# Kernel tuning notes

Hardware: AMD Instinct MI355X
Metric: run time of the kernel (lower is better)

Reference implementation:

```python
import jax, jax.numpy as jnp
import numpy as np

NUM_EMBEDDINGS = 1024
EMBEDDING_DIM = 256
BETA = 0.25


def setup_inputs() -> dict:
    key = jax.random.key(0)
    k1, k2 = jax.random.split(key)
    inputs = jax.random.normal(k1, (32, EMBEDDING_DIM, 64, 64), dtype=jnp.float32)
    # codebook init: uniform(-1/K, 1/K), matching nn.Embedding init in the module
    embedding = jax.random.uniform(
        k2, (NUM_EMBEDDINGS, EMBEDDING_DIM), dtype=jnp.float32,
        minval=-1.0 / NUM_EMBEDDINGS, maxval=1.0 / NUM_EMBEDDINGS)
    return {"inputs": inputs, "embedding": embedding, "beta": BETA}


def reference(inputs, embedding, beta):
    # inputs: [B, D, H, W] -> [B, H, W, D]
    x = jnp.transpose(inputs, (0, 2, 3, 1))
    in_shape = x.shape
    flat = x.reshape(-1, embedding.shape[1])  # [N, D]
    dist = (jnp.sum(flat * flat, axis=1, keepdims=True)
            + jnp.sum(embedding * embedding, axis=1)
            - 2.0 * flat @ embedding.T)
    codebook_indices = jnp.argmin(dist, axis=1)  # [N]
    quantized = embedding[codebook_indices].reshape(in_shape)  # [B,H,W,D]
    sg = jax.lax.stop_gradient
    e_latent_loss = beta * jnp.mean((sg(quantized) - x) ** 2)
    q_latent_loss = jnp.mean((quantized - sg(x)) ** 2)
    loss = e_latent_loss + q_latent_loss
    # straight-through estimator
    quantized_st = x + sg(quantized - x)
    return loss, jnp.transpose(quantized_st, (0, 3, 1, 2))
```

## Files before the change

kernel.cpp:

```cpp
#include <hip/hip_runtime.h>
#include <hip/hip_bf16.h>


#define DIN 256
#define NCODES 1024
#define NTOT 33554432

typedef __attribute__((ext_vector_type(8))) short short8;
typedef __attribute__((ext_vector_type(4))) float float4v;
typedef __attribute__((ext_vector_type(4))) unsigned short ushort4v;

static __device__ __forceinline__ unsigned short f2bf(float f) {
  unsigned int u = __float_as_uint(f);
  unsigned int r = (u + 0x7fffu + ((u >> 16) & 1u)) >> 16;
  return (unsigned short)r;
}

__global__ void vq_prep(const float* __restrict__ e,
                        unsigned short* __restrict__ e_bf,
                        float* __restrict__ norms) {
  int wave = threadIdx.x >> 6, lane = threadIdx.x & 63;
  int k = blockIdx.x * 4 + wave;
  const float4v* src = (const float4v*)(e + k * DIN);
  float4v v = src[lane];
  float ss = v[0]*v[0] + v[1]*v[1] + v[2]*v[2] + v[3]*v[3];
  ushort4v pk;
  pk[0] = f2bf(v[0]); pk[1] = f2bf(v[1]); pk[2] = f2bf(v[2]); pk[3] = f2bf(v[3]);
  ((ushort4v*)(e_bf + k * DIN))[lane] = pk;
  #pragma unroll
  for (int m = 1; m < 64; m <<= 1) ss += __shfl_xor(ss, m, 64);
  if (lane == 0) norms[k] = ss;
}

__global__ void __launch_bounds__(256, 2)
vq_main(const float* __restrict__ xin, const float* __restrict__ e_fp,
        const unsigned short* __restrict__ e_bf, const float* __restrict__ norms,
        float* __restrict__ out, float* __restrict__ loss_acc) {
  __shared__ char smem[65536];
  unsigned short* xs = (unsigned short*)smem;
  unsigned short* es = (unsigned short*)smem;
  float* vs  = (float*)(smem + 49152);
  int*   is_ = (int*)  (smem + 49664);
  int*   fi  = (int*)  (smem + 50176);
  float* rs  = (float*)(smem + 50432);
  float* qs  = (float*)smem;

  const int tid  = threadIdx.x;
  const int wave = tid >> 6, lane = tid & 63;
  const int m16  = lane & 15, quad = lane >> 4;
  const int wr   = wave >> 1, wc = wave & 1;
  const int b    = blockIdx.x >> 6, h = blockIdx.x & 63;
  const int base = b * 1048576 + h * 64;

  {
    int w = lane;
    for (int q8 = 0; q8 < 8; ++q8) {
      int cc = q8 * 4 + wave;
      int d0 = cc * 8;
      short8 pk;
      #pragma unroll
      for (int ii = 0; ii < 8; ++ii) {
        float xv = xin[base + (d0 + ii) * 4096 + w];
        pk[ii] = (short)f2bf(xv);
      }
      *(short8*)(xs + w * 256 + 8 * (cc ^ (w & 7))) = pk;
    }
  }
  __syncthreads();

  short8 areg[16];
  #pragma unroll
  for (int i = 0; i < 2; ++i) {
    #pragma unroll
    for (int kk = 0; kk < 8; ++kk) {
      int r = wr * 32 + i * 16 + m16;
      int cc = kk * 4 + quad;
      areg[i * 8 + kk] = *(short8*)(xs + r * 256 + 8 * (cc ^ (r & 7)));
    }
  }
  __syncthreads();

  float bestv[2][4];
  int   besti[2][4];
  float4v acc[2][4];
  #pragma unroll
  for (int i = 0; i < 2; ++i)
    #pragma unroll
    for (int r = 0; r < 4; ++r) {
      bestv[i][r] = INFINITY; besti[i][r] = 0;
      acc[i][r] = (float4v)(0.0f);
    }

  for (int ct = 0; ct < 8; ++ct) {
    int c0 = ct * 128;
    #pragma unroll
    for (int j = 0; j < 16; ++j) {
      int f = j * 256 + tid;
      int kL = f >> 5, cc = f & 31;
      short8 vch = *(const short8*)(e_bf + (c0 + kL) * 256 + cc * 8);
      *(short8*)(es + kL * 256 + 8 * (cc ^ (kL & 7))) = vch;
    }
    __syncthreads();
    #pragma unroll
    for (int kk = 0; kk < 8; ++kk) {
      short8 bfr[4];
      #pragma unroll
      for (int j = 0; j < 4; ++j) {
        int cL = wc * 64 + j * 16 + m16;
        int cc = kk * 4 + quad;
        bfr[j] = *(short8*)(es + cL * 256 + 8 * (cc ^ (cL & 7)));
      }
      #pragma unroll
      for (int i = 0; i < 2; ++i)
        #pragma unroll
        for (int j = 0; j < 4; ++j)
          acc[i][j] = __builtin_amdgcn_mfma_f32_16x16x32_bf16(
              areg[i * 8 + kk], bfr[j], acc[i][j], 0, 0, 0);
    }
    #pragma unroll
    for (int j = 0; j < 4; ++j) {
      int col = c0 + wc * 64 + j * 16 + m16;
      float nj = norms[col];
      #pragma unroll
      for (int i = 0; i < 2; ++i) {
        #pragma unroll
        for (int r = 0; r < 4; ++r) {
          float s = nj - 2.0f * acc[i][j][r];
          if (s < bestv[i][r]) { bestv[i][r] = s; besti[i][r] = col; }
        }
        acc[i][j] = (float4v)(0.0f);
      }
    }
    __syncthreads();
  }

  #pragma unroll
  for (int msk = 1; msk <= 8; msk <<= 1) {
    #pragma unroll
    for (int i = 0; i < 2; ++i)
      #pragma unroll
      for (int r = 0; r < 4; ++r) {
        float ov = __shfl_xor(bestv[i][r], msk, 64);
        int   oi = __shfl_xor(besti[i][r], msk, 64);
        if (ov < bestv[i][r] || (ov == bestv[i][r] && oi < besti[i][r])) {
          bestv[i][r] = ov; besti[i][r] = oi;
        }
      }
  }
  if (m16 == 0) {
    #pragma unroll
    for (int i = 0; i < 2; ++i)
      #pragma unroll
      for (int r = 0; r < 4; ++r) {
        int rl = wr * 32 + i * 16 + quad * 4 + r;
        vs [rl * 2 + wc] = bestv[i][r];
        is_[rl * 2 + wc] = besti[i][r];
      }
  }
  __syncthreads();
  if (tid < 64) {
    float v0 = vs[tid * 2], v1 = vs[tid * 2 + 1];
    fi[tid] = (v1 < v0) ? is_[tid * 2 + 1] : is_[tid * 2];
  }
  __syncthreads();

  float lsum = 0.0f;
  for (int h2 = 0; h2 < 2; ++h2) {
    #pragma unroll
    for (int j = 0; j < 8; ++j) {
      int f = j * 256 + tid;
      int w2 = f >> 5, cc = f & 31;
      int idx = fi[w2];
      float4v qv = *(const float4v*)(e_fp + idx * DIN + h2 * 128 + cc * 4);
      #pragma unroll
      for (int ii = 0; ii < 4; ++ii)
        qs[(cc * 4 + ii) * 65 + w2] = qv[ii];
    }
    __syncthreads();
    for (int dd = 0; dd < 32; ++dd) {
      int dL = wave * 32 + dd;
      int g = base + (h2 * 128 + dL) * 4096 + lane;
      float q  = qs[dL * 65 + lane];
      float xv = xin[g];
      out[1 + g] = q;
      float df = q - xv;
      lsum += df * df;
    }
    __syncthreads();
  }

  #pragma unroll
  for (int msk = 1; msk < 64; msk <<= 1) lsum += __shfl_xor(lsum, msk, 64);
  if (lane == 0) rs[wave] = lsum;
  __syncthreads();
  if (tid == 0) atomicAdd(loss_acc, rs[0] + rs[1] + rs[2] + rs[3]);
}

__global__ void vq_fin(const float* __restrict__ loss_acc,
                       const float* __restrict__ beta,
                       float* __restrict__ out) {
  out[0] = (1.0f + beta[0]) * loss_acc[0] / 33554432.0f;
}

extern "C" void kernel_launch(void* const* d_in, const int* in_sizes, int n_in,
                              void* d_out, int out_size, void* d_ws, size_t ws_size,
                              hipStream_t stream) {
  const float* xin  = (const float*)d_in[0];
  const float* emb  = (const float*)d_in[1];
  const float* beta = (const float*)d_in[2];
  float* out = (float*)d_out;
  float* loss_acc = (float*)d_ws;
  float* norms = (float*)((char*)d_ws + 4096);
  unsigned short* e_bf = (unsigned short*)((char*)d_ws + 8192);

  hipMemsetAsync(d_ws, 0, 4, stream);
  vq_prep<<<256, 256, 0, stream>>>(emb, e_bf, norms);
  vq_main<<<2048, 256, 0, stream>>>(xin, emb, e_bf, norms, out, loss_acc);
  vq_fin<<<1, 1, 0, stream>>>(loss_acc, beta, out);
}
```

Before: 364.2 us.

## Chunk-major codebook layout with direct-to-LDS loads, smaller tiles for higher occupancy

```diff
diff --git a/kernel.cpp b/kernel.cpp
--- a/kernel.cpp
+++ b/kernel.cpp
@@ -4,10 +4,10 @@
 
 #define DIN 256
 #define NCODES 1024
-#define NTOT 33554432
 
 typedef __attribute__((ext_vector_type(8))) short short8;
 typedef __attribute__((ext_vector_type(4))) float float4v;
+typedef __attribute__((ext_vector_type(2))) float float2v;
 typedef __attribute__((ext_vector_type(4))) unsigned short ushort4v;
 
 static __device__ __forceinline__ unsigned short f2bf(float f) {
@@ -17,33 +17,32 @@
 }
 
 __global__ void vq_prep(const float* __restrict__ e,
-                        unsigned short* __restrict__ e_bf,
+                        unsigned short* __restrict__ e_bf2,
                         float* __restrict__ norms) {
   int wave = threadIdx.x >> 6, lane = threadIdx.x & 63;
   int k = blockIdx.x * 4 + wave;
-  const float4v* src = (const float4v*)(e + k * DIN);
-  float4v v = src[lane];
+  float4v v = ((const float4v*)(e + k * DIN))[lane];
   float ss = v[0]*v[0] + v[1]*v[1] + v[2]*v[2] + v[3]*v[3];
   ushort4v pk;
   pk[0] = f2bf(v[0]); pk[1] = f2bf(v[1]); pk[2] = f2bf(v[2]); pk[3] = f2bf(v[3]);
-  ((ushort4v*)(e_bf + k * DIN))[lane] = pk;
+  int cc = lane >> 1, sub = lane & 1;
+  *(ushort4v*)(e_bf2 + (cc * NCODES + k) * 8 + sub * 4) = pk;
   #pragma unroll
   for (int m = 1; m < 64; m <<= 1) ss += __shfl_xor(ss, m, 64);
   if (lane == 0) norms[k] = ss;
 }
 
-__global__ void __launch_bounds__(256, 2)
+__global__ void __launch_bounds__(256, 4)
 vq_main(const float* __restrict__ xin, const float* __restrict__ e_fp,
-        const unsigned short* __restrict__ e_bf, const float* __restrict__ norms,
+        const unsigned short* __restrict__ e_bf2, const float* __restrict__ norms,
         float* __restrict__ out, float* __restrict__ loss_acc) {
-  __shared__ char smem[65536];
-  unsigned short* xs = (unsigned short*)smem;
+  __shared__ char smem[34080];
   unsigned short* es = (unsigned short*)smem;
-  float* vs  = (float*)(smem + 49152);
-  int*   is_ = (int*)  (smem + 49664);
-  int*   fi  = (int*)  (smem + 50176);
-  float* rs  = (float*)(smem + 50432);
   float* qs  = (float*)smem;
+  float* vs  = (float*)(smem + 32768);
+  int*   is_ = (int*)  (smem + 33280);
+  int*   fi  = (int*)  (smem + 33792);
+  float* rs  = (float*)(smem + 34048);
 
   const int tid  = threadIdx.x;
   const int wave = tid >> 6, lane = tid & 63;
@@ -52,74 +51,57 @@
   const int b    = blockIdx.x >> 6, h = blockIdx.x & 63;
   const int base = b * 1048576 + h * 64;
 
-  {
-    int w = lane;
-    for (int q8 = 0; q8 < 8; ++q8) {
-      int cc = q8 * 4 + wave;
-      int d0 = cc * 8;
+  short8 areg[16];
+  #pragma unroll
+  for (int i = 0; i < 2; ++i) {
+    int r = wr * 32 + i * 16 + m16;
+    #pragma unroll
+    for (int kk = 0; kk < 8; ++kk) {
+      int cc = kk * 4 + quad;
       short8 pk;
       #pragma unroll
-      for (int ii = 0; ii < 8; ++ii) {
-        float xv = xin[base + (d0 + ii) * 4096 + w];
-        pk[ii] = (short)f2bf(xv);
-      }
-      *(short8*)(xs + w * 256 + 8 * (cc ^ (w & 7))) = pk;
-    }
-  }
-  __syncthreads();
-
-  short8 areg[16];
-  #pragma unroll
-  for (int i = 0; i < 2; ++i) {
-    #pragma unroll
-    for (int kk = 0; kk < 8; ++kk) {
-      int r = wr * 32 + i * 16 + m16;
-      int cc = kk * 4 + quad;
-      areg[i * 8 + kk] = *(short8*)(xs + r * 256 + 8 * (cc ^ (r & 7)));
-    }
-  }
-  __syncthreads();
+      for (int ii = 0; ii < 8; ++ii)
+        pk[ii] = (short)f2bf(xin[base + (cc * 8 + ii) * 4096 + r]);
+      areg[i * 8 + kk] = pk;
+    }
+  }
 
   float bestv[2][4];
   int   besti[2][4];
-  float4v acc[2][4];
-  #pragma unroll
-  for (int i = 0; i < 2; ++i)
-    #pragma unroll
-    for (int r = 0; r < 4; ++r) {
-      bestv[i][r] = INFINITY; besti[i][r] = 0;
-      acc[i][r] = (float4v)(0.0f);
-    }
-
-  for (int ct = 0; ct < 8; ++ct) {
-    int c0 = ct * 128;
-    #pragma unroll
-    for (int j = 0; j < 16; ++j) {
-      int f = j * 256 + tid;
-      int kL = f >> 5, cc = f & 31;
-      short8 vch = *(const short8*)(e_bf + (c0 + kL) * 256 + cc * 8);
-      *(short8*)(es + kL * 256 + 8 * (cc ^ (kL & 7))) = vch;
+  float4v acc[2][2];
+  #pragma unroll
+  for (int i = 0; i < 2; ++i) {
+    #pragma unroll
+    for (int r = 0; r < 4; ++r) { bestv[i][r] = INFINITY; besti[i][r] = 0; }
+    #pragma unroll
+    for (int j = 0; j < 2; ++j) acc[i][j] = (float4v)(0.0f);
+  }
+
+  for (int ct = 0; ct < 16; ++ct) {
+    int c0 = ct * 64;
+    #pragma unroll
+    for (int q = 0; q < 8; ++q) {
+      int cc8 = wave * 8 + q;
+      const unsigned short* gsrc = e_bf2 + (cc8 * NCODES + c0) * 8 + lane * 8;
+      unsigned short* ldst = es + cc8 * 512;
+      __builtin_amdgcn_global_load_lds(
+          (const __attribute__((address_space(1))) void*)gsrc,
+          (__attribute__((address_space(3))) void*)ldst, 16, 0, 0);
     }
     __syncthreads();
     #pragma unroll
     for (int kk = 0; kk < 8; ++kk) {
-      short8 bfr[4];
-      #pragma unroll
-      for (int j = 0; j < 4; ++j) {
-        int cL = wc * 64 + j * 16 + m16;
-        int cc = kk * 4 + quad;
-        bfr[j] = *(short8*)(es + cL * 256 + 8 * (cc ^ (cL & 7)));
-      }
-      #pragma unroll
-      for (int i = 0; i < 2; ++i)
-        #pragma unroll
-        for (int j = 0; j < 4; ++j)
-          acc[i][j] = __builtin_amdgcn_mfma_f32_16x16x32_bf16(
-              areg[i * 8 + kk], bfr[j], acc[i][j], 0, 0, 0);
-    }
-    #pragma unroll
-    for (int j = 0; j < 4; ++j) {
-      int col = c0 + wc * 64 + j * 16 + m16;
+      int cc = kk * 4 + quad;
+      short8 b0 = *(short8*)(es + (cc * 64 + wc * 32 + m16) * 8);
+      short8 b1 = *(short8*)(es + (cc * 64 + wc * 32 + 16 + m16) * 8);
+      acc[0][0] = __builtin_amdgcn_mfma_f32_16x16x32_bf16(areg[kk],     b0, acc[0][0], 0, 0, 0);
+      acc[0][1] = __builtin_amdgcn_mfma_f32_16x16x32_bf16(areg[kk],     b1, acc[0][1], 0, 0, 0);
+      acc[1][0] = __builtin_amdgcn_mfma_f32_16x16x32_bf16(areg[8 + kk], b0, acc[1][0], 0, 0, 0);
+      acc[1][1] = __builtin_amdgcn_mfma_f32_16x16x32_bf16(areg[8 + kk], b1, acc[1][1], 0, 0, 0);
+    }
+    #pragma unroll
+    for (int j = 0; j < 2; ++j) {
+      int col = c0 + wc * 32 + j * 16 + m16;
       float nj = norms[col];
       #pragma unroll
       for (int i = 0; i < 2; ++i) {
@@ -160,31 +142,35 @@
   __syncthreads();
   if (tid < 64) {
     float v0 = vs[tid * 2], v1 = vs[tid * 2 + 1];
-    fi[tid] = (v1 < v0) ? is_[tid * 2 + 1] : is_[tid * 2];
+    int   i0 = is_[tid * 2], i1 = is_[tid * 2 + 1];
+    fi[tid] = (v1 < v0 || (v1 == v0 && i1 < i0)) ? i1 : i0;
   }
   __syncthreads();
 
   float lsum = 0.0f;
-  for (int h2 = 0; h2 < 2; ++h2) {
-    #pragma unroll
-    for (int j = 0; j < 8; ++j) {
+  const int wq = tid & 31, dL0 = tid >> 5;
+  for (int h2 = 0; h2 < 4; ++h2) {
+    #pragma unroll
+    for (int j = 0; j < 4; ++j) {
       int f = j * 256 + tid;
-      int w2 = f >> 5, cc = f & 31;
+      int w2 = f >> 4, cc = f & 15;
       int idx = fi[w2];
-      float4v qv = *(const float4v*)(e_fp + idx * DIN + h2 * 128 + cc * 4);
+      float4v qv = *(const float4v*)(e_fp + idx * DIN + h2 * 64 + cc * 4);
       #pragma unroll
       for (int ii = 0; ii < 4; ++ii)
-        qs[(cc * 4 + ii) * 65 + w2] = qv[ii];
-    }
-    __syncthreads();
-    for (int dd = 0; dd < 32; ++dd) {
-      int dL = wave * 32 + dd;
-      int g = base + (h2 * 128 + dL) * 4096 + lane;
-      float q  = qs[dL * 65 + lane];
-      float xv = xin[g];
-      out[1 + g] = q;
-      float df = q - xv;
-      lsum += df * df;
+        qs[(cc * 4 + ii) * 66 + w2] = qv[ii];
+    }
+    __syncthreads();
+    #pragma unroll
+    for (int dd = 0; dd < 8; ++dd) {
+      int dL = dd * 8 + dL0;
+      int g = base + (h2 * 64 + dL) * 4096 + wq * 2;
+      float2v q  = *(float2v*)(qs + dL * 66 + wq * 2);
+      float2v xv = *(const float2v*)(xin + g);
+      out[1 + g] = q[0];
+      out[2 + g] = q[1];
+      float d0 = q[0] - xv[0], d1 = q[1] - xv[1];
+      lsum += d0 * d0 + d1 * d1;
     }
     __syncthreads();
   }
@@ -211,10 +197,10 @@
   float* out = (float*)d_out;
   float* loss_acc = (float*)d_ws;
   float* norms = (float*)((char*)d_ws + 4096);
-  unsigned short* e_bf = (unsigned short*)((char*)d_ws + 8192);
+  unsigned short* e_bf2 = (unsigned short*)((char*)d_ws + 8192);
 
   hipMemsetAsync(d_ws, 0, 4, stream);
-  vq_prep<<<256, 256, 0, stream>>>(emb, e_bf, norms);
-  vq_main<<<2048, 256, 0, stream>>>(xin, emb, e_bf, norms, out, loss_acc);
+  vq_prep<<<256, 256, 0, stream>>>(emb, e_bf2, norms);
+  vq_main<<<2048, 256, 0, stream>>>(xin, emb, e_bf2, norms, out, loss_acc);
   vq_fin<<<1, 1, 0, stream>>>(loss_acc, beta, out);
 }
```

After: 365.3 us. Within noise of the previous version (+0.3%).
